# Optimization experiments

Hardware: AMD Instinct MI355X
Metric: run time of the kernel (lower is better)

The kernel has to match this reference:

```python
import jax, jax.numpy as jnp
import numpy as np
import math

D_MODEL = 768
NUM_HEADS = 12
D_K = D_MODEL // NUM_HEADS

def setup_inputs() -> dict:
    key = jax.random.key(0)
    k_x, k_q, k_k, k_v, k_o = jax.random.split(key, 5)
    x = jax.random.normal(k_x, (2, 2048, D_MODEL), dtype=jnp.float32)
    std = math.sqrt(2.0 / (D_MODEL + D_MODEL))
    # trunc_normal approx: clip normal to [-3std, 3std]
    def tn(k):
        return jnp.clip(jax.random.normal(k, (D_MODEL, D_MODEL), dtype=jnp.float32) * std, -3 * std, 3 * std)
    return {
        "x": x,
        "weight_query": tn(k_q),
        "weight_key": tn(k_k),
        "weight_value": tn(k_v),
        "weight_output": tn(k_o),
    }

def reference(x, weight_query, weight_key, weight_value, weight_output):
    # x: (b, s, d_model); weights: (d_out, d_model)
    b, s, _ = x.shape
    def proj_heads(w):
        y = jnp.einsum('od,bsd->bso', w, x)  # (b, s, h*dk)
        return y.reshape(b, s, NUM_HEADS, D_K).transpose(0, 2, 1, 3)  # (b, h, s, dk)
    Q = proj_heads(weight_query)
    K = proj_heads(weight_key)
    V = proj_heads(weight_value)
    scores = jnp.einsum('bhqd,bhkd->bhqk', Q, K) / jnp.sqrt(jnp.asarray(D_K, x.dtype))
    causal = jnp.tril(jnp.ones((s, s), dtype=bool))  # (sq, sk)
    scores = jnp.where(causal, scores, -jnp.inf)
    attn = jax.nn.softmax(scores, axis=-1)
    out_heads = jnp.einsum('bhqk,bhkd->bhqd', attn, V)  # (b, h, s, dv)
    attn_out = out_heads.transpose(0, 2, 1, 3).reshape(b, s, NUM_HEADS * D_K)
    return jnp.einsum('di,bsi->bsd', weight_output, attn_out)
```

## Files before the change

kernel.cpp:

```cpp
#include <hip/hip_runtime.h>
#include <stdint.h>

typedef float f32x4 __attribute__((ext_vector_type(4)));
typedef __bf16 bf16x8 __attribute__((ext_vector_type(8)));
typedef uint32_t u32a  __attribute__((may_alias));
typedef uint2    u2a   __attribute__((may_alias));
typedef uint4    u4a   __attribute__((may_alias));

#define VS 2064

__device__ __forceinline__ ushort f2b(float f) {
  uint32_t u = __builtin_bit_cast(uint32_t, f);
  u += 0x7FFFu + ((u >> 16) & 1u);
  return (ushort)(u >> 16);
}
__device__ __forceinline__ uint32_t b16(uint32_t u) {
  u += 0x7FFFu + ((u >> 16) & 1u);
  return u >> 16;
}

__device__ __forceinline__ bf16x8 ld_frag(const ushort* p) {
  u4a u = *(const u4a*)p;
  return __builtin_bit_cast(bf16x8, u);
}

__device__ __forceinline__ u4a cvt8(const float* p) {
  u4a a = *(const u4a*)p, b = *(const u4a*)(p + 4), o;
  o.x = b16(a.x) | (b16(a.y) << 16);
  o.y = b16(a.z) | (b16(a.w) << 16);
  o.z = b16(b.x) | (b16(b.y) << 16);
  o.w = b16(b.z) | (b16(b.w) << 16);
  return o;
}

__device__ __forceinline__ void load_lds16(const void* g, void* l) {
  __builtin_amdgcn_global_load_lds(
      (const __attribute__((address_space(1))) uint32_t*)g,
      (__attribute__((address_space(3))) uint32_t*)l, 16, 0, 0);
}

__device__ __forceinline__ uint32_t comb2(uint32_t a, uint32_t b, float w0, float w1) {
  float lo = __builtin_bit_cast(float, a << 16) * w0 +
             __builtin_bit_cast(float, b << 16) * w1;
  float hi = __builtin_bit_cast(float, a & 0xFFFF0000u) * w0 +
             __builtin_bit_cast(float, b & 0xFFFF0000u) * w1;
  return (uint32_t)f2b(lo) | ((uint32_t)f2b(hi) << 16);
}

__global__ __launch_bounds__(256) void convert_kernel(
    const float* __restrict__ x,  const float* __restrict__ wq,
    const float* __restrict__ wk, const float* __restrict__ wv,
    const float* __restrict__ wo,
    ushort* __restrict__ xb,  ushort* __restrict__ wqb,
    ushort* __restrict__ wkb, ushort* __restrict__ wvb,
    ushort* __restrict__ wob)
{
  const size_t NX = 3145728, NW = 589824;
  size_t idx = ((size_t)blockIdx.x * 256 + threadIdx.x) * 8;
  const float* src; ushort* dst; size_t off;
  if      (idx < NX)          { src = x;  dst = xb;  off = idx; }
  else if (idx < NX + NW)     { src = wq; dst = wqb; off = idx - NX; }
  else if (idx < NX + 2 * NW) { src = wk; dst = wkb; off = idx - NX - NW; }
  else if (idx < NX + 3 * NW) { src = wv; dst = wvb; off = idx - NX - 2 * NW; }
  else                        { src = wo; dst = wob; off = idx - NX - 3 * NW; }
  *(u4a*)(dst + off) = cvt8(src + off);
}

__global__ __launch_bounds__(256) void gemm_qkv(
    const ushort* __restrict__ A,
    const ushort* __restrict__ B0, const ushort* __restrict__ B1,
    const ushort* __restrict__ B2,
    ushort* __restrict__ Qo, ushort* __restrict__ Ko, ushort* __restrict__ Vt,
    int M, int N, int K)
{
  const ushort* B = blockIdx.z == 0 ? B0 : (blockIdx.z == 1 ? B1 : B2);
  const int m0 = blockIdx.x * 128, n0 = blockIdx.y * 64;
  __shared__ ushort As[128 * 64];
  __shared__ ushort Bs[64 * 64];
  const int tid = threadIdx.x, wave = tid >> 6, lane = tid & 63;
  const int quad = lane >> 4, l16 = lane & 15;
  const int mw = (wave & 1) * 64, nw = (wave >> 1) * 32;
  f32x4 acc[4][2] = {};

  for (int k0 = 0; k0 < K; k0 += 64) {
#pragma unroll
    for (int i = 0; i < 4; ++i) {
      int c = i * 256 + tid;
      load_lds16(A + (size_t)(m0 + (c >> 3)) * K + k0 + (c & 7) * 8,
                 As + (size_t)(i * 256 + wave * 64) * 8);
    }
#pragma unroll
    for (int i = 0; i < 2; ++i) {
      int c = i * 256 + tid;
      load_lds16(B + (size_t)(n0 + (c >> 3)) * K + k0 + (c & 7) * 8,
                 Bs + (size_t)(i * 256 + wave * 64) * 8);
    }
    __syncthreads();
#pragma unroll
    for (int ks = 0; ks < 2; ++ks) {
      bf16x8 af[4], bfr[2];
#pragma unroll
      for (int i = 0; i < 4; ++i)
        af[i]  = ld_frag(As + (mw + i * 16 + l16) * 64 + ks * 32 + quad * 8);
#pragma unroll
      for (int j = 0; j < 2; ++j)
        bfr[j] = ld_frag(Bs + (nw + j * 16 + l16) * 64 + ks * 32 + quad * 8);
#pragma unroll
      for (int i = 0; i < 4; ++i)
#pragma unroll
        for (int j = 0; j < 2; ++j)
          acc[i][j] = __builtin_amdgcn_mfma_f32_16x16x32_bf16(af[i], bfr[j], acc[i][j], 0, 0, 0);
    }
    __syncthreads();
  }
  if (blockIdx.z < 2) {
    ushort* C = blockIdx.z == 0 ? Qo : Ko;
    const float sc = blockIdx.z == 0 ? 0.125f : 1.0f;
#pragma unroll
    for (int i = 0; i < 4; ++i)
#pragma unroll
      for (int j = 0; j < 2; ++j)
#pragma unroll
        for (int r = 0; r < 4; ++r) {
          int row = m0 + mw + i * 16 + quad * 4 + r;
          int col = n0 + nw + j * 16 + l16;
          C[(size_t)row * N + col] = f2b(acc[i][j][r] * sc);
        }
  } else {
#pragma unroll
    for (int i = 0; i < 4; ++i)
#pragma unroll
      for (int j = 0; j < 2; ++j) {
        int col = n0 + nw + j * 16 + l16;
        int h = col >> 6, dv = col & 63;
        int t = m0 + mw + i * 16 + quad * 4;
        int b = t >> 11, s = t & 2047;
        u2a pw;
        pw.x = (uint32_t)f2b(acc[i][j][0]) | ((uint32_t)f2b(acc[i][j][1]) << 16);
        pw.y = (uint32_t)f2b(acc[i][j][2]) | ((uint32_t)f2b(acc[i][j][3]) << 16);
        *(u2a*)(Vt + (((size_t)b * 12 + h) * 64 + dv) * VS + s) = pw;
      }
  }
}

__global__ __launch_bounds__(256) void gemm_out(
    const ushort* __restrict__ A, const ushort* __restrict__ B,
    float* __restrict__ C, int M, int N, int K)
{
  const int m0 = blockIdx.x * 64, n0 = blockIdx.y * 64;
  __shared__ ushort As[64 * 64];
  __shared__ ushort Bs[64 * 64];
  const int tid = threadIdx.x, wave = tid >> 6, lane = tid & 63;
  const int quad = lane >> 4, l16 = lane & 15;
  const int mw = (wave & 1) * 32, nw = (wave >> 1) * 32;
  f32x4 acc[2][2] = {};

  for (int k0 = 0; k0 < K; k0 += 64) {
#pragma unroll
    for (int i = 0; i < 2; ++i) {
      int c = i * 256 + tid;
      load_lds16(A + (size_t)(m0 + (c >> 3)) * K + k0 + (c & 7) * 8,
                 As + (size_t)(i * 256 + wave * 64) * 8);
      load_lds16(B + (size_t)(n0 + (c >> 3)) * K + k0 + (c & 7) * 8,
                 Bs + (size_t)(i * 256 + wave * 64) * 8);
    }
    __syncthreads();
#pragma unroll
    for (int ks = 0; ks < 2; ++ks) {
      bf16x8 af[2], bfr[2];
#pragma unroll
      for (int i = 0; i < 2; ++i)
        af[i]  = ld_frag(As + (mw + i * 16 + l16) * 64 + ks * 32 + quad * 8);
#pragma unroll
      for (int j = 0; j < 2; ++j)
        bfr[j] = ld_frag(Bs + (nw + j * 16 + l16) * 64 + ks * 32 + quad * 8);
#pragma unroll
      for (int i = 0; i < 2; ++i)
#pragma unroll
        for (int j = 0; j < 2; ++j)
          acc[i][j] = __builtin_amdgcn_mfma_f32_16x16x32_bf16(af[i], bfr[j], acc[i][j], 0, 0, 0);
    }
    __syncthreads();
  }
#pragma unroll
  for (int i = 0; i < 2; ++i)
#pragma unroll
    for (int j = 0; j < 2; ++j)
#pragma unroll
      for (int r = 0; r < 4; ++r) {
        int row = m0 + mw + i * 16 + quad * 4 + r;
        int col = n0 + nw + j * 16 + l16;
        C[(size_t)row * N + col] = acc[i][j][r];
      }
}

__global__ __launch_bounds__(256) void attn_kernel(
    const ushort* __restrict__ Qb, const ushort* __restrict__ Kb,
    const ushort* __restrict__ Vt, ushort* __restrict__ Opart,
    float2* __restrict__ MLp)
{
  const int S = 2048, DM = 768;
  const int pair = blockIdx.x >> 1, j = blockIdx.x & 1;
  const int h = blockIdx.y, bb = blockIdx.z;
  const ushort* Qp  = Qb + (size_t)bb * S * DM + h * 64;
  const ushort* Kp  = Kb + (size_t)bb * S * DM + h * 64;
  const ushort* Vth = Vt + ((size_t)bb * 12 + h) * 64 * VS;

  __shared__ ushort Ks[128 * 72];
  __shared__ ushort Vs[64 * 136];
  __shared__ ushort Ps[4][16 * 136];

  const int tid = threadIdx.x, wave = tid >> 6, lane = tid & 63;
  const int quad = lane >> 4, l16 = lane & 15;
  const float LOG2E = 1.44269504f;
  const float NEG_BIG = -1.0e30f;

  const int qtA = pair, qtB = 31 - pair;
  const int qgA = qtA * 64 + wave * 16 + l16;
  const int qgB = qtB * 64 + wave * 16 + l16;
  const int nktA = (qtA >> 1) + 1, nktB = (qtB >> 1) + 1;

  bf16x8 bqA0 = ld_frag(Qp + (size_t)qgA * DM + quad * 8);
  bf16x8 bqA1 = ld_frag(Qp + (size_t)qgA * DM + 32 + quad * 8);
  bf16x8 bqB0 = ld_frag(Qp + (size_t)qgB * DM + quad * 8);
  bf16x8 bqB1 = ld_frag(Qp + (size_t)qgB * DM + 32 + quad * 8);

  f32x4 accA[4] = {}, accB[4] = {};
  float mA = NEG_BIG, lA = 0.0f, mB = NEG_BIG, lB = 0.0f;

  for (int kt = j; kt < nktB; kt += 2) {
    const int kk0 = kt * 128;
#pragma unroll
    for (int i = 0; i < 4; ++i) {
      int c = i * 256 + tid;
      int r = c >> 3, col = (c & 7) * 8;
      *(u4a*)(Ks + r * 72 + col) = *(const u4a*)(Kp + (size_t)(kk0 + r) * DM + col);
    }
#pragma unroll
    for (int i = 0; i < 4; ++i) {
      int c = i * 256 + tid;
      int dv = c >> 4, kc = (c & 15) * 8;
      *(u4a*)(Vs + dv * 136 + kc) = *(const u4a*)(Vth + (size_t)dv * VS + kk0 + kc);
    }
    __syncthreads();

    auto strip = [&](const bf16x8& bq0, const bf16x8& bq1, f32x4* acc_o,
                     float& m_run, float& l_run, int qg, int nkt) {
      f32x4 sacc[8] = {};
#pragma unroll
      for (int tt = 0; tt < 8; ++tt) {
        bf16x8 ak0 = ld_frag(Ks + (tt * 16 + l16) * 72 + quad * 8);
        bf16x8 ak1 = ld_frag(Ks + (tt * 16 + l16) * 72 + 32 + quad * 8);
        sacc[tt] = __builtin_amdgcn_mfma_f32_16x16x32_bf16(ak0, bq0, sacc[tt], 0, 0, 0);
        sacc[tt] = __builtin_amdgcn_mfma_f32_16x16x32_bf16(ak1, bq1, sacc[tt], 0, 0, 0);
      }
      const bool domask = (kt == nkt - 1);
      float mt = NEG_BIG;
#pragma unroll
      for (int tt = 0; tt < 8; ++tt)
#pragma unroll
        for (int r = 0; r < 4; ++r) {
          float s = sacc[tt][r];
          if (domask) {
            int kkg = kk0 + tt * 16 + quad * 4 + r;
            if (kkg > qg) s = NEG_BIG;
          }
          sacc[tt][r] = s;
          mt = fmaxf(mt, s);
        }
      mt = fmaxf(mt, __shfl_xor(mt, 16, 64));
      mt = fmaxf(mt, __shfl_xor(mt, 32, 64));
      float mnew = fmaxf(m_run, mt);
      float alpha = exp2f((m_run - mnew) * LOG2E);
      float lsum = 0.0f;
#pragma unroll
      for (int tt = 0; tt < 8; ++tt) {
        float p0 = exp2f((sacc[tt][0] - mnew) * LOG2E);
        float p1 = exp2f((sacc[tt][1] - mnew) * LOG2E);
        float p2 = exp2f((sacc[tt][2] - mnew) * LOG2E);
        float p3 = exp2f((sacc[tt][3] - mnew) * LOG2E);
        lsum += (p0 + p1) + (p2 + p3);
        uint32_t u0 = __builtin_bit_cast(uint32_t, p0);
        uint32_t u1 = __builtin_bit_cast(uint32_t, p1);
        uint32_t u2 = __builtin_bit_cast(uint32_t, p2);
        uint32_t u3 = __builtin_bit_cast(uint32_t, p3);
        u2a pw;
        pw.x = (u0 >> 16) | (u1 & 0xFFFF0000u);
        pw.y = (u2 >> 16) | (u3 & 0xFFFF0000u);
        *(u2a*)(&Ps[wave][l16 * 136 + tt * 16 + quad * 4]) = pw;
      }
      asm volatile("s_waitcnt lgkmcnt(0)" ::: "memory");
      lsum += __shfl_xor(lsum, 16, 64);
      lsum += __shfl_xor(lsum, 32, 64);
      l_run = l_run * alpha + lsum;
      m_run = mnew;
      float ar0 = __shfl(alpha, quad * 4 + 0, 64);
      float ar1 = __shfl(alpha, quad * 4 + 1, 64);
      float ar2 = __shfl(alpha, quad * 4 + 2, 64);
      float ar3 = __shfl(alpha, quad * 4 + 3, 64);
#pragma unroll
      for (int ct = 0; ct < 4; ++ct) {
        acc_o[ct][0] *= ar0; acc_o[ct][1] *= ar1;
        acc_o[ct][2] *= ar2; acc_o[ct][3] *= ar3;
      }
#pragma unroll
      for (int ks = 0; ks < 4; ++ks) {
        bf16x8 ap = ld_frag(&Ps[wave][l16 * 136 + ks * 32 + quad * 8]);
#pragma unroll
        for (int ct = 0; ct < 4; ++ct) {
          bf16x8 bv = ld_frag(Vs + (size_t)(ct * 16 + l16) * 136 + ks * 32 + quad * 8);
          acc_o[ct] = __builtin_amdgcn_mfma_f32_16x16x32_bf16(ap, bv, acc_o[ct], 0, 0, 0);
        }
      }
    };

    strip(bqB0, bqB1, accB, mB, lB, qgB, nktB);
    if (kt < nktA)
      strip(bqA0, bqA1, accA, mA, lA, qgA, nktA);
    __syncthreads();
  }

  const int base = ((bb * 12 + h) << 5);
  const int r0 = wave * 16 + quad * 4;
  {
    const int slot = (base + qtB) * 2 + j;
    ushort* Os = Opart + (size_t)slot * 4096;
#pragma unroll
    for (int ct = 0; ct < 4; ++ct) {
      int col = ct * 16 + l16;
      Os[(r0 + 0) * 64 + col] = f2b(accB[ct][0]);
      Os[(r0 + 1) * 64 + col] = f2b(accB[ct][1]);
      Os[(r0 + 2) * 64 + col] = f2b(accB[ct][2]);
      Os[(r0 + 3) * 64 + col] = f2b(accB[ct][3]);
    }
    if (quad == 0)
      MLp[(size_t)slot * 64 + wave * 16 + l16] = make_float2(mB, lB);
  }
  {
    const int slot = (base + qtA) * 2 + j;
    ushort* Os = Opart + (size_t)slot * 4096;
#pragma unroll
    for (int ct = 0; ct < 4; ++ct) {
      int col = ct * 16 + l16;
      Os[(r0 + 0) * 64 + col] = f2b(accA[ct][0]);
      Os[(r0 + 1) * 64 + col] = f2b(accA[ct][1]);
      Os[(r0 + 2) * 64 + col] = f2b(accA[ct][2]);
      Os[(r0 + 3) * 64 + col] = f2b(accA[ct][3]);
    }
    if (quad == 0)
      MLp[(size_t)slot * 64 + wave * 16 + l16] = make_float2(mA, lA);
  }
}

__global__ __launch_bounds__(256) void combine_kernel(
    const ushort* __restrict__ Opart, const float2* __restrict__ MLp,
    ushort* __restrict__ Ab)
{
  const int sid = blockIdx.x;
  const int bb = sid / 384, rem = sid % 384, h = rem >> 5, qt = rem & 31;
  const int t = threadIdx.x, row = t >> 2, cg = (t & 3) * 16;
  float2 ml0 = MLp[(size_t)(sid * 2) * 64 + row];
  float2 ml1 = MLp[(size_t)(sid * 2 + 1) * 64 + row];
  float ms = fmaxf(ml0.x, ml1.x);
  float w0 = exp2f((ml0.x - ms) * 1.44269504f);
  float w1 = exp2f((ml1.x - ms) * 1.44269504f);
  float inv = 1.0f / (ml0.y * w0 + ml1.y * w1);
  w0 *= inv; w1 *= inv;
  const ushort* p0 = Opart + (size_t)(sid * 2) * 4096 + row * 64 + cg;
  ushort* dst = Ab + ((size_t)(bb * 2048 + qt * 64 + row)) * 768 + h * 64 + cg;
#pragma unroll
  for (int g = 0; g < 2; ++g) {
    u4a a = *(const u4a*)(p0 + g * 8);
    u4a b = *(const u4a*)(p0 + 4096 + g * 8);
    u4a o;
    o.x = comb2(a.x, b.x, w0, w1);
    o.y = comb2(a.y, b.y, w0, w1);
    o.z = comb2(a.z, b.z, w0, w1);
    o.w = comb2(a.w, b.w, w0, w1);
    *(u4a*)(dst + g * 8) = o;
  }
}

extern "C" void kernel_launch(void* const* d_in, const int* in_sizes, int n_in,
                              void* d_out, int out_size, void* d_ws, size_t ws_size,
                              hipStream_t stream) {
  (void)in_sizes; (void)n_in; (void)out_size; (void)ws_size;
  const float* x  = (const float*)d_in[0];
  const float* wq = (const float*)d_in[1];
  const float* wk = (const float*)d_in[2];
  const float* wv = (const float*)d_in[3];
  const float* wo = (const float*)d_in[4];

  const size_t NT = (size_t)4096 * 768;
  const size_t NW = (size_t)768 * 768;
  const size_t NV = (size_t)24 * 64 * VS;
  ushort* xb    = (ushort*)d_ws;
  ushort* Qbuf  = xb + NT;
  ushort* Kbuf  = Qbuf + NT;
  ushort* Vt    = Kbuf + NT;
  ushort* wqb   = Vt + NV;
  ushort* wkb   = wqb + NW;
  ushort* wvb   = wkb + NW;
  ushort* wob   = wvb + NW;
  ushort* Opart = wob + NW;
  float2* MLp   = (float2*)(Opart + (size_t)1536 * 4096);
  ushort* Abuf  = xb;

  convert_kernel<<<2688, 256, 0, stream>>>(x, wq, wk, wv, wo,
                                           xb, wqb, wkb, wvb, wob);
  gemm_qkv<<<dim3(32, 12, 3), 256, 0, stream>>>(
      xb, wqb, wkb, wvb, Qbuf, Kbuf, Vt, 4096, 768, 768);
  attn_kernel<<<dim3(32, 12, 2), 256, 0, stream>>>(Qbuf, Kbuf, Vt, Opart, MLp);
  combine_kernel<<<768, 256, 0, stream>>>(Opart, MLp, Abuf);
  gemm_out<<<dim3(64, 12), 256, 0, stream>>>(
      Abuf, wob, (float*)d_out, 4096, 768, 768);
}
```

Baseline: 173.0 us.

## Register-prefetch next tiles in GEMMs and attention, pad GEMM LDS rows

In both GEMMs and the attention loop, the next K-tile is now loaded from global memory into registers right after the barrier, so the load overlaps the MFMA work on the current tile. The GEMMs stop using direct global-to-LDS loads and instead store through registers into LDS rows padded to 68 elements, which is meant to cut bank conflicts on fragment reads. The cost is more registers per thread, which may lower occupancy, and an extra register-to-LDS store step.

```diff
diff --git a/kernel.cpp b/kernel.cpp
--- a/kernel.cpp
+++ b/kernel.cpp
@@ -8,6 +8,7 @@
 typedef uint4    u4a   __attribute__((may_alias));
 
 #define VS 2064
+#define GS 68
 
 __device__ __forceinline__ ushort f2b(float f) {
   uint32_t u = __builtin_bit_cast(uint32_t, f);
@@ -31,12 +32,6 @@
   o.z = b16(b.x) | (b16(b.y) << 16);
   o.w = b16(b.z) | (b16(b.w) << 16);
   return o;
-}
-
-__device__ __forceinline__ void load_lds16(const void* g, void* l) {
-  __builtin_amdgcn_global_load_lds(
-      (const __attribute__((address_space(1))) uint32_t*)g,
-      (__attribute__((address_space(3))) uint32_t*)l, 16, 0, 0);
 }
 
 __device__ __forceinline__ uint32_t comb2(uint32_t a, uint32_t b, float w0, float w1) {
@@ -75,36 +70,50 @@
 {
   const ushort* B = blockIdx.z == 0 ? B0 : (blockIdx.z == 1 ? B1 : B2);
   const int m0 = blockIdx.x * 128, n0 = blockIdx.y * 64;
-  __shared__ ushort As[128 * 64];
-  __shared__ ushort Bs[64 * 64];
+  __shared__ ushort As[128 * GS];
+  __shared__ ushort Bs[64 * GS];
   const int tid = threadIdx.x, wave = tid >> 6, lane = tid & 63;
   const int quad = lane >> 4, l16 = lane & 15;
   const int mw = (wave & 1) * 64, nw = (wave >> 1) * 32;
   f32x4 acc[4][2] = {};
 
+  u4a pa[4], pb[2];
+  auto fetch = [&](int k0) {
+#pragma unroll
+    for (int i = 0; i < 4; ++i) {
+      int c = i * 256 + tid;
+      pa[i] = *(const u4a*)(A + (size_t)(m0 + (c >> 3)) * K + k0 + (c & 7) * 8);
+    }
+#pragma unroll
+    for (int i = 0; i < 2; ++i) {
+      int c = i * 256 + tid;
+      pb[i] = *(const u4a*)(B + (size_t)(n0 + (c >> 3)) * K + k0 + (c & 7) * 8);
+    }
+  };
+  fetch(0);
+
   for (int k0 = 0; k0 < K; k0 += 64) {
 #pragma unroll
     for (int i = 0; i < 4; ++i) {
       int c = i * 256 + tid;
-      load_lds16(A + (size_t)(m0 + (c >> 3)) * K + k0 + (c & 7) * 8,
-                 As + (size_t)(i * 256 + wave * 64) * 8);
+      *(u4a*)(As + (c >> 3) * GS + (c & 7) * 8) = pa[i];
     }
 #pragma unroll
     for (int i = 0; i < 2; ++i) {
       int c = i * 256 + tid;
-      load_lds16(B + (size_t)(n0 + (c >> 3)) * K + k0 + (c & 7) * 8,
-                 Bs + (size_t)(i * 256 + wave * 64) * 8);
-    }
-    __syncthreads();
+      *(u4a*)(Bs + (c >> 3) * GS + (c & 7) * 8) = pb[i];
+    }
+    __syncthreads();
+    if (k0 + 64 < K) fetch(k0 + 64);
 #pragma unroll
     for (int ks = 0; ks < 2; ++ks) {
       bf16x8 af[4], bfr[2];
 #pragma unroll
       for (int i = 0; i < 4; ++i)
-        af[i]  = ld_frag(As + (mw + i * 16 + l16) * 64 + ks * 32 + quad * 8);
+        af[i]  = ld_frag(As + (mw + i * 16 + l16) * GS + ks * 32 + quad * 8);
 #pragma unroll
       for (int j = 0; j < 2; ++j)
-        bfr[j] = ld_frag(Bs + (nw + j * 16 + l16) * 64 + ks * 32 + quad * 8);
+        bfr[j] = ld_frag(Bs + (nw + j * 16 + l16) * GS + ks * 32 + quad * 8);
 #pragma unroll
       for (int i = 0; i < 4; ++i)
 #pragma unroll
@@ -148,32 +157,42 @@
     float* __restrict__ C, int M, int N, int K)
 {
   const int m0 = blockIdx.x * 64, n0 = blockIdx.y * 64;
-  __shared__ ushort As[64 * 64];
-  __shared__ ushort Bs[64 * 64];
+  __shared__ ushort As[64 * GS];
+  __shared__ ushort Bs[64 * GS];
   const int tid = threadIdx.x, wave = tid >> 6, lane = tid & 63;
   const int quad = lane >> 4, l16 = lane & 15;
   const int mw = (wave & 1) * 32, nw = (wave >> 1) * 32;
   f32x4 acc[2][2] = {};
 
+  u4a pa[2], pb[2];
+  auto fetch = [&](int k0) {
+#pragma unroll
+    for (int i = 0; i < 2; ++i) {
+      int c = i * 256 + tid;
+      pa[i] = *(const u4a*)(A + (size_t)(m0 + (c >> 3)) * K + k0 + (c & 7) * 8);
+      pb[i] = *(const u4a*)(B + (size_t)(n0 + (c >> 3)) * K + k0 + (c & 7) * 8);
+    }
+  };
+  fetch(0);
+
   for (int k0 = 0; k0 < K; k0 += 64) {
 #pragma unroll
     for (int i = 0; i < 2; ++i) {
       int c = i * 256 + tid;
-      load_lds16(A + (size_t)(m0 + (c >> 3)) * K + k0 + (c & 7) * 8,
-                 As + (size_t)(i * 256 + wave * 64) * 8);
-      load_lds16(B + (size_t)(n0 + (c >> 3)) * K + k0 + (c & 7) * 8,
-                 Bs + (size_t)(i * 256 + wave * 64) * 8);
-    }
-    __syncthreads();
+      *(u4a*)(As + (c >> 3) * GS + (c & 7) * 8) = pa[i];
+      *(u4a*)(Bs + (c >> 3) * GS + (c & 7) * 8) = pb[i];
+    }
+    __syncthreads();
+    if (k0 + 64 < K) fetch(k0 + 64);
 #pragma unroll
     for (int ks = 0; ks < 2; ++ks) {
       bf16x8 af[2], bfr[2];
 #pragma unroll
       for (int i = 0; i < 2; ++i)
-        af[i]  = ld_frag(As + (mw + i * 16 + l16) * 64 + ks * 32 + quad * 8);
+        af[i]  = ld_frag(As + (mw + i * 16 + l16) * GS + ks * 32 + quad * 8);
 #pragma unroll
       for (int j = 0; j < 2; ++j)
-        bfr[j] = ld_frag(Bs + (nw + j * 16 + l16) * 64 + ks * 32 + quad * 8);
+        bfr[j] = ld_frag(Bs + (nw + j * 16 + l16) * GS + ks * 32 + quad * 8);
 #pragma unroll
       for (int i = 0; i < 2; ++i)
 #pragma unroll
@@ -228,21 +247,28 @@
   f32x4 accA[4] = {}, accB[4] = {};
   float mA = NEG_BIG, lA = 0.0f, mB = NEG_BIG, lB = 0.0f;
 
+  u4a kr[4], vr[4];
+  auto fetch_tile = [&](int kt) {
+    const int kk0 = kt * 128;
+#pragma unroll
+    for (int i = 0; i < 4; ++i) {
+      int c = i * 256 + tid;
+      kr[i] = *(const u4a*)(Kp + (size_t)(kk0 + (c >> 3)) * DM + (c & 7) * 8);
+      vr[i] = *(const u4a*)(Vth + (size_t)(c >> 4) * VS + kk0 + (c & 15) * 8);
+    }
+  };
+  fetch_tile(j);
+
   for (int kt = j; kt < nktB; kt += 2) {
     const int kk0 = kt * 128;
 #pragma unroll
     for (int i = 0; i < 4; ++i) {
       int c = i * 256 + tid;
-      int r = c >> 3, col = (c & 7) * 8;
-      *(u4a*)(Ks + r * 72 + col) = *(const u4a*)(Kp + (size_t)(kk0 + r) * DM + col);
-    }
-#pragma unroll
-    for (int i = 0; i < 4; ++i) {
-      int c = i * 256 + tid;
-      int dv = c >> 4, kc = (c & 15) * 8;
-      *(u4a*)(Vs + dv * 136 + kc) = *(const u4a*)(Vth + (size_t)dv * VS + kk0 + kc);
-    }
-    __syncthreads();
+      *(u4a*)(Ks + (c >> 3) * 72 + (c & 7) * 8) = kr[i];
+      *(u4a*)(Vs + (c >> 4) * 136 + (c & 15) * 8) = vr[i];
+    }
+    __syncthreads();
+    if (kt + 2 < nktB) fetch_tile(kt + 2);
 
     auto strip = [&](const bf16x8& bq0, const bf16x8& bq1, f32x4* acc_o,
                      float& m_run, float& l_run, int qg, int nkt) {
```

Measured after the change: 348.0 us. 2.01x slower.

## Register-prefetch next tiles in GEMMs and attention, pad GEMM LDS rows

Applied to the files above, without the earlier changes.

Replaces the direct global-to-LDS loads in both GEMM kernels, and the synchronous K/V tile loads in attention, with register prefetching. The next tile's global loads are issued right after the barrier so they overlap with the current tile's MFMA work. GEMM LDS rows are also padded from 64 to 68 elements to cut bank conflicts on fragment reads. In exchange it uses more registers, which may reduce occupancy, and it gives up the async LDS-load path.

```diff
diff --git a/kernel.cpp b/kernel.cpp
--- a/kernel.cpp
+++ b/kernel.cpp
@@ -8,6 +8,7 @@
 typedef uint4    u4a   __attribute__((may_alias));
 
 #define VS 2064
+#define GS 68
 
 __device__ __forceinline__ ushort f2b(float f) {
   uint32_t u = __builtin_bit_cast(uint32_t, f);
@@ -31,12 +32,6 @@
   o.z = b16(b.x) | (b16(b.y) << 16);
   o.w = b16(b.z) | (b16(b.w) << 16);
   return o;
-}
-
-__device__ __forceinline__ void load_lds16(const void* g, void* l) {
-  __builtin_amdgcn_global_load_lds(
-      (const __attribute__((address_space(1))) uint32_t*)g,
-      (__attribute__((address_space(3))) uint32_t*)l, 16, 0, 0);
 }
 
 __device__ __forceinline__ uint32_t comb2(uint32_t a, uint32_t b, float w0, float w1) {
@@ -75,36 +70,47 @@
 {
   const ushort* B = blockIdx.z == 0 ? B0 : (blockIdx.z == 1 ? B1 : B2);
   const int m0 = blockIdx.x * 128, n0 = blockIdx.y * 64;
-  __shared__ ushort As[128 * 64];
-  __shared__ ushort Bs[64 * 64];
+  __shared__ ushort As[128 * GS];
+  __shared__ ushort Bs[64 * GS];
   const int tid = threadIdx.x, wave = tid >> 6, lane = tid & 63;
   const int quad = lane >> 4, l16 = lane & 15;
   const int mw = (wave & 1) * 64, nw = (wave >> 1) * 32;
+  const int rr = tid >> 3, cc = (tid & 7) * 8;
+  const ushort* Ag = A + (size_t)(m0 + rr) * K + cc;
+  const ushort* Bg = B + (size_t)(n0 + rr) * K + cc;
+  const size_t a32 = (size_t)32 * K;
+  ushort* Al = As + rr * GS + cc;
+  ushort* Bl = Bs + rr * GS + cc;
   f32x4 acc[4][2] = {};
 
+  u4a pa0, pa1, pa2, pa3, pb0, pb1;
+#define QKV_FETCH(k0_)                                   \
+  pa0 = *(const u4a*)(Ag + (k0_));                       \
+  pa1 = *(const u4a*)(Ag + (k0_) + a32);                 \
+  pa2 = *(const u4a*)(Ag + (k0_) + 2 * a32);             \
+  pa3 = *(const u4a*)(Ag + (k0_) + 3 * a32);             \
+  pb0 = *(const u4a*)(Bg + (k0_));                       \
+  pb1 = *(const u4a*)(Bg + (k0_) + a32);
+  QKV_FETCH(0)
+
   for (int k0 = 0; k0 < K; k0 += 64) {
-#pragma unroll
-    for (int i = 0; i < 4; ++i) {
-      int c = i * 256 + tid;
-      load_lds16(A + (size_t)(m0 + (c >> 3)) * K + k0 + (c & 7) * 8,
-                 As + (size_t)(i * 256 + wave * 64) * 8);
-    }
-#pragma unroll
-    for (int i = 0; i < 2; ++i) {
-      int c = i * 256 + tid;
-      load_lds16(B + (size_t)(n0 + (c >> 3)) * K + k0 + (c & 7) * 8,
-                 Bs + (size_t)(i * 256 + wave * 64) * 8);
-    }
-    __syncthreads();
+    *(u4a*)(Al)               = pa0;
+    *(u4a*)(Al + 32 * GS)     = pa1;
+    *(u4a*)(Al + 64 * GS)     = pa2;
+    *(u4a*)(Al + 96 * GS)     = pa3;
+    *(u4a*)(Bl)               = pb0;
+    *(u4a*)(Bl + 32 * GS)     = pb1;
+    __syncthreads();
+    if (k0 + 64 < K) { QKV_FETCH(k0 + 64) }
 #pragma unroll
     for (int ks = 0; ks < 2; ++ks) {
       bf16x8 af[4], bfr[2];
 #pragma unroll
       for (int i = 0; i < 4; ++i)
-        af[i]  = ld_frag(As + (mw + i * 16 + l16) * 64 + ks * 32 + quad * 8);
+        af[i]  = ld_frag(As + (mw + i * 16 + l16) * GS + ks * 32 + quad * 8);
 #pragma unroll
       for (int j = 0; j < 2; ++j)
-        bfr[j] = ld_frag(Bs + (nw + j * 16 + l16) * 64 + ks * 32 + quad * 8);
+        bfr[j] = ld_frag(Bs + (nw + j * 16 + l16) * GS + ks * 32 + quad * 8);
 #pragma unroll
       for (int i = 0; i < 4; ++i)
 #pragma unroll
@@ -113,6 +119,7 @@
     }
     __syncthreads();
   }
+#undef QKV_FETCH
   if (blockIdx.z < 2) {
     ushort* C = blockIdx.z == 0 ? Qo : Ko;
     const float sc = blockIdx.z == 0 ? 0.125f : 1.0f;
@@ -148,32 +155,43 @@
     float* __restrict__ C, int M, int N, int K)
 {
   const int m0 = blockIdx.x * 64, n0 = blockIdx.y * 64;
-  __shared__ ushort As[64 * 64];
-  __shared__ ushort Bs[64 * 64];
+  __shared__ ushort As[64 * GS];
+  __shared__ ushort Bs[64 * GS];
   const int tid = threadIdx.x, wave = tid >> 6, lane = tid & 63;
   const int quad = lane >> 4, l16 = lane & 15;
   const int mw = (wave & 1) * 32, nw = (wave >> 1) * 32;
+  const int rr = tid >> 3, cc = (tid & 7) * 8;
+  const ushort* Ag = A + (size_t)(m0 + rr) * K + cc;
+  const ushort* Bg = B + (size_t)(n0 + rr) * K + cc;
+  const size_t a32 = (size_t)32 * K;
+  ushort* Al = As + rr * GS + cc;
+  ushort* Bl = Bs + rr * GS + cc;
   f32x4 acc[2][2] = {};
 
+  u4a pa0, pa1, pb0, pb1;
+#define OUT_FETCH(k0_)                                   \
+  pa0 = *(const u4a*)(Ag + (k0_));                       \
+  pa1 = *(const u4a*)(Ag + (k0_) + a32);                 \
+  pb0 = *(const u4a*)(Bg + (k0_));                       \
+  pb1 = *(const u4a*)(Bg + (k0_) + a32);
+  OUT_FETCH(0)
+
   for (int k0 = 0; k0 < K; k0 += 64) {
-#pragma unroll
-    for (int i = 0; i < 2; ++i) {
-      int c = i * 256 + tid;
-      load_lds16(A + (size_t)(m0 + (c >> 3)) * K + k0 + (c & 7) * 8,
-                 As + (size_t)(i * 256 + wave * 64) * 8);
-      load_lds16(B + (size_t)(n0 + (c >> 3)) * K + k0 + (c & 7) * 8,
-                 Bs + (size_t)(i * 256 + wave * 64) * 8);
-    }
-    __syncthreads();
+    *(u4a*)(Al)           = pa0;
+    *(u4a*)(Al + 32 * GS) = pa1;
+    *(u4a*)(Bl)           = pb0;
+    *(u4a*)(Bl + 32 * GS) = pb1;
+    __syncthreads();
+    if (k0 + 64 < K) { OUT_FETCH(k0 + 64) }
 #pragma unroll
     for (int ks = 0; ks < 2; ++ks) {
       bf16x8 af[2], bfr[2];
 #pragma unroll
       for (int i = 0; i < 2; ++i)
-        af[i]  = ld_frag(As + (mw + i * 16 + l16) * 64 + ks * 32 + quad * 8);
+        af[i]  = ld_frag(As + (mw + i * 16 + l16) * GS + ks * 32 + quad * 8);
 #pragma unroll
       for (int j = 0; j < 2; ++j)
-        bfr[j] = ld_frag(Bs + (nw + j * 16 + l16) * 64 + ks * 32 + quad * 8);
+        bfr[j] = ld_frag(Bs + (nw + j * 16 + l16) * GS + ks * 32 + quad * 8);
 #pragma unroll
       for (int i = 0; i < 2; ++i)
 #pragma unroll
@@ -182,6 +200,7 @@
     }
     __syncthreads();
   }
+#undef OUT_FETCH
 #pragma unroll
   for (int i = 0; i < 2; ++i)
 #pragma unroll
@@ -228,21 +247,40 @@
   f32x4 accA[4] = {}, accB[4] = {};
   float mA = NEG_BIG, lA = 0.0f, mB = NEG_BIG, lB = 0.0f;
 
+  const int krr = tid >> 3, kcc = (tid & 7) * 8;
+  const int vrr = tid >> 4, vcc = (tid & 15) * 8;
+  const ushort* Kg = Kp + (size_t)krr * DM + kcc;
+  const size_t k32 = (size_t)32 * DM;
+  const ushort* Vg = Vth + (size_t)vrr * VS + vcc;
+  const size_t v16 = (size_t)16 * VS;
+  ushort* Kl = Ks + krr * 72 + kcc;
+  ushort* Vl = Vs + vrr * 136 + vcc;
+
+  u4a kr0, kr1, kr2, kr3, vr0, vr1, vr2, vr3;
+#define ATTN_FETCH(kt_) {                                        \
+  const size_t o = (size_t)(kt_) * 128;                          \
+  kr0 = *(const u4a*)(Kg + o * DM);                              \
+  kr1 = *(const u4a*)(Kg + o * DM + k32);                        \
+  kr2 = *(const u4a*)(Kg + o * DM + 2 * k32);                    \
+  kr3 = *(const u4a*)(Kg + o * DM + 3 * k32);                    \
+  vr0 = *(const u4a*)(Vg + o);                                   \
+  vr1 = *(const u4a*)(Vg + o + v16);                             \
+  vr2 = *(const u4a*)(Vg + o + 2 * v16);                         \
+  vr3 = *(const u4a*)(Vg + o + 3 * v16); }
+  ATTN_FETCH(j)
+
   for (int kt = j; kt < nktB; kt += 2) {
     const int kk0 = kt * 128;
-#pragma unroll
-    for (int i = 0; i < 4; ++i) {
-      int c = i * 256 + tid;
-      int r = c >> 3, col = (c & 7) * 8;
-      *(u4a*)(Ks + r * 72 + col) = *(const u4a*)(Kp + (size_t)(kk0 + r) * DM + col);
-    }
-#pragma unroll
-    for (int i = 0; i < 4; ++i) {
-      int c = i * 256 + tid;
-      int dv = c >> 4, kc = (c & 15) * 8;
-      *(u4a*)(Vs + dv * 136 + kc) = *(const u4a*)(Vth + (size_t)dv * VS + kk0 + kc);
-    }
-    __syncthreads();
+    *(u4a*)(Kl)            = kr0;
+    *(u4a*)(Kl + 32 * 72)  = kr1;
+    *(u4a*)(Kl + 64 * 72)  = kr2;
+    *(u4a*)(Kl + 96 * 72)  = kr3;
+    *(u4a*)(Vl)            = vr0;
+    *(u4a*)(Vl + 16 * 136) = vr1;
+    *(u4a*)(Vl + 32 * 136) = vr2;
+    *(u4a*)(Vl + 48 * 136) = vr3;
+    __syncthreads();
+    if (kt + 2 < nktB) ATTN_FETCH(kt + 2)
 
     auto strip = [&](const bf16x8& bq0, const bf16x8& bq1, f32x4* acc_o,
                      float& m_run, float& l_run, int qg, int nkt) {
@@ -319,6 +357,7 @@
       strip(bqA0, bqA1, accA, mA, lA, qgA, nktA);
     __syncthreads();
   }
+#undef ATTN_FETCH
 
   const int base = ((bb * 12 + h) << 5);
   const int r0 = wave * 16 + quad * 4;
```

Result: slower. 278.7 us (+61.1%).
